# Optimization experiments

Measured on AMD Instinct MI355X. Metric: run time of the kernel, lower is better.

Reference implementation:

```python
import jax, jax.numpy as jnp
import numpy as np

CH = 64
HEADS = 4
HD = CH // HEADS          # 16
BLOCK = 8
HALO = 1
NEIGH = BLOCK + 2 * HALO  # 10
SR = 2
HDH = HD // 2             # 8


def conv1x1(x, w, b=None):
    y = jnp.einsum('oc,bchw->bohw', w, x)
    return y if b is None else y + b[None, :, None, None]


def dw3x3(x, w, pad_mode):
    # depthwise 3x3 conv, padding=1 with given pad mode
    xp = jnp.pad(x, ((0, 0), (0, 0), (1, 1), (1, 1)), mode=pad_mode)
    return jax.lax.conv_general_dilated(
        xp, w, (1, 1), 'VALID',
        dimension_numbers=('NCHW', 'OIHW', 'NCHW'),
        feature_group_count=x.shape[1])


def maxpool2(x):
    return jax.lax.reduce_window(x, -jnp.inf, jax.lax.max, (1, 1, 2, 2), (1, 1, 2, 2), 'VALID')


def l2norm(x):
    return x / jnp.maximum(jnp.linalg.norm(x, axis=-1, keepdims=True), 1e-12)


def sorted_channel_indices(q):
    # correlation-based channel ordering (computed under no_grad in torch)
    B, C = q.shape[0], q.shape[1]
    f = jax.lax.stop_gradient(q.reshape(B, C, -1))
    cen = f - f.mean(axis=2, keepdims=True)
    cov = jnp.einsum('bcn,bdn->bcd', cen, cen)
    std = jnp.sqrt(jnp.diagonal(cov, axis1=1, axis2=2) + 1e-8)
    denom = jnp.maximum(std[:, :, None] * std[:, None, :], 1e-8)
    sim = (cov / denom).mean(axis=2)
    return jnp.argsort(-sim, axis=1)  # descending


def up_bilinear_ac(x, s):
    # bilinear upsample, align_corners=True (torch convention)
    def lerp_axis(t, axis):
        n_in = t.shape[axis]
        n_out = n_in * s
        c = jnp.arange(n_out, dtype=t.dtype) * ((n_in - 1.0) / (n_out - 1.0))
        lo = jnp.clip(jnp.floor(c).astype(jnp.int32), 0, n_in - 2)
        w = c - lo.astype(t.dtype)
        shape = [1] * t.ndim
        shape[axis] = n_out
        w = w.reshape(shape)
        return jnp.take(t, lo, axis=axis) * (1 - w) + jnp.take(t, lo + 1, axis=axis) * w
    return lerp_axis(lerp_axis(x, 2), 3)


def _forward(x, qkv_w, lce_w, gate_w, gate_b, temp, rel_h_emb, rel_w_emb,
             down_w, down_b, up_w, up_b, gating_w, gating_b, proj_w, lp_w, lp_b):
    x_in = maxpool2(x)                         # sr=2 sampler
    B, C, H, W = x_in.shape                    # H,W divisible by BLOCK -> no pad branch
    hb, wb = H // BLOCK, W // BLOCK
    BL = B * hb * wb

    qkv = dw3x3(conv1x1(x_in, qkv_w), lce_w, 'constant')   # qkv_conv + lce
    q, k, v = jnp.split(qkv, 3, axis=1)

    idx = sorted_channel_indices(q)
    gidx = idx[:, :, None, None]
    q_s = jnp.take_along_axis(q, gidx, axis=1)
    k_s = jnp.take_along_axis(k, gidx, axis=1)
    v_s = jnp.take_along_axis(v, gidx, axis=1)

    # gating: grouped 1x1 conv, one [HD,HD] matmul per head
    qh = q_s.reshape(B, HEADS, HD, H, W)
    gate_score = jnp.einsum('goc,bgcxy->bgoxy', gate_w, qh) + gate_b[None, :, :, None, None]

    # query blocks: [BL, heads, block*block, hd]
    qi = qh.reshape(B, HEADS, HD, hb, BLOCK, wb, BLOCK)
    qi = qi.transpose(0, 3, 5, 1, 4, 6, 2).reshape(BL, HEADS, BLOCK * BLOCK, HD)

    def halo_patches(t):
        # F.unfold(kernel=NEIGH, stride=BLOCK, padding=HALO), zero pad
        tp = jnp.pad(t, ((0, 0), (0, 0), (HALO, HALO), (HALO, HALO)))
        ridx = jnp.arange(hb)[:, None] * BLOCK + jnp.arange(NEIGH)[None, :]
        cidx = jnp.arange(wb)[:, None] * BLOCK + jnp.arange(NEIGH)[None, :]
        p = tp[:, :, ridx, :][..., cidx]       # [B, C, hb, NEIGH, wb, NEIGH]
        p = p.reshape(B, HEADS, HD, hb, NEIGH, wb, NEIGH).transpose(0, 3, 5, 1, 4, 6, 2)
        return p.reshape(BL, HEADS, NEIGH, NEIGH, HD)

    ks = halo_patches(k_s)
    vi = halo_patches(v_s).reshape(BL, HEADS, NEIGH * NEIGH, HD)

    # relative positional embeddings on split key channels
    kh = ks[..., :HDH] + rel_h_emb             # [BL,heads,NEIGH,NEIGH,HDH]
    kw = ks[..., HDH:] + rel_w_emb
    ki = jnp.concatenate([kh, kw], axis=-1).reshape(BL, HEADS, NEIGH * NEIGH, HD)

    logits = jnp.einsum('bhqc,bhkc->bhqk', l2norm(qi), l2norm(ki)) * jnp.exp(temp)
    attn = jax.nn.softmax(logits, axis=-1)
    out_i = jnp.einsum('bhqk,bhkc->bhqc', attn, vi)

    out = out_i.reshape(B, hb, wb, HEADS, BLOCK, BLOCK, HD)
    out = out.transpose(0, 3, 6, 1, 4, 2, 5).reshape(B, HEADS, HD, H, W)
    out = (out * jax.nn.sigmoid(gate_score)).reshape(B, C, H, W)

    cache = q_s + k_s
    inv = jnp.argsort(idx, axis=1)[:, :, None, None]
    out = jnp.take_along_axis(out, inv, axis=1)
    cache = jnp.take_along_axis(cache, inv, axis=1)

    # Intra_CacheModulation
    mixed = out + cache
    g = jax.nn.gelu(conv1x1(mixed, gating_w, gating_b), approximate=False) * mixed
    out = out + conv1x1(conv1x1(g, down_w, down_b), up_w, up_b)

    out = conv1x1(out, proj_w)
    # LocalProp: depthwise 3x3 reflect-pad conv + bilinear x2 (align_corners=True)
    out = dw3x3(out, lp_w, 'reflect') + lp_b[None, :, None, None]
    out = up_bilinear_ac(out, SR)
    # final F.interpolate to input size is identity here (shapes already match)
    return out


def setup_inputs() -> dict:
    key = jax.random.key(0)
    ks = jax.random.split(key, 12)
    B, H, W = 4, 256, 256
    p = lambda k, shape, s=0.02: jax.random.normal(k, shape, jnp.float32) * s
    return {
        'x': jax.random.normal(ks[0], (B, CH, H, W), jnp.float32),
        'qkv_w': p(ks[1], (3 * CH, CH), 0.05),
        'lce_w': p(ks[2], (3 * CH, 1, 3, 3), 0.1),
        'gate_w': p(ks[3], (HEADS, HD, HD), 0.1),
        'gate_b': jnp.ones((HEADS, HD), jnp.float32),
        'temp': jnp.zeros((1, HEADS, 1, 1), jnp.float32),
        'rel_h_emb': p(ks[4], (1, HEADS, NEIGH, 1, HDH)),
        'rel_w_emb': p(ks[5], (1, HEADS, 1, NEIGH, HD - HDH)),
        'down_w': p(ks[6], (CH // 2, CH), 0.05),
        'down_b': jnp.zeros((CH // 2,), jnp.float32),
        'up_w': p(ks[7], (CH, CH // 2), 0.05),
        'up_b': jnp.zeros((CH,), jnp.float32),
        'gating_w': p(ks[8], (CH, CH), 0.05),
        'gating_b': jnp.zeros((CH,), jnp.float32),
        'proj_w': p(ks[9], (CH, CH), 0.05),
        'lp_w': p(ks[10], (CH, 1, 3, 3), 0.1),
        'lp_b': jnp.zeros((CH,), jnp.float32),
    }


def reference(x, qkv_w, lce_w, gate_w, gate_b, temp, rel_h_emb, rel_w_emb,
              down_w, down_b, up_w, up_b, gating_w, gating_b, proj_w, lp_w, lp_b):
    return _forward(x, qkv_w, lce_w, gate_w, gate_b, temp, rel_h_emb, rel_w_emb,
                    down_w, down_b, up_w, up_b, gating_w, gating_b, proj_w, lp_w, lp_b)
```

## Files before the change

kernel.cpp:

```cpp
#include <hip/hip_runtime.h>
#include <math.h>

#define HWP 16384

typedef float f32x2 __attribute__((ext_vector_type(2)));
typedef float f32x4 __attribute__((ext_vector_type(4)));

static __device__ __forceinline__ f32x2 pk_fma(f32x2 a, f32x2 b, f32x2 c) {
  f32x2 d;
  asm("v_pk_fma_f32 %0, %1, %2, %3" : "=v"(d) : "v"(a), "v"(b), "v"(c));
  return d;
}

static const size_t PRE_OFF  = 0;
static const size_t QKV_OFF  = 12582912;
static const size_t WT_OFF   = QKV_OFF;
static const size_t COVP_OFF = 0;
static const size_t MEAN_OFF = 2097152;
static const size_t COVS_OFF = 2097408;
static const size_t ATTN_OFF = 0;
static const size_t OUT3_OFF = 4194304;
static const size_t IDX_OFF  = 12570112;
static const size_t INV_OFF  = 12570368;
static const size_t GT2_OFF  = 12570624;
static const size_t DT2_OFF  = 12574720;
static const size_t UT2_OFF  = 12576768;
static const size_t PT2_OFF  = 12578816;

__global__ __launch_bounds__(256) void k_prep_wt(
    const float* __restrict__ qkv_w, float* __restrict__ wT) {
  int i = blockIdx.x * 256 + threadIdx.x;
  int o = i >> 6, c = i & 63;
  wT[c * 192 + o] = qkv_w[i];
}

__global__ __launch_bounds__(256) void k_prep2(
    const float* __restrict__ gating_w, const float* __restrict__ down_w,
    const float* __restrict__ up_w, const float* __restrict__ proj_w,
    float* __restrict__ gT, float* __restrict__ dT,
    float* __restrict__ uT, float* __restrict__ pT) {
  int t = blockIdx.x * 256 + threadIdx.x;
  if (t < 4096) {
    int o = t >> 6, d = t & 63;
    gT[d * 64 + o] = gating_w[t];
    pT[d * 64 + o] = proj_w[t];
  }
  if (t < 2048) {
    int o = t >> 6, d = t & 63;
    dT[d * 32 + o] = down_w[t];
    int o2 = t >> 5, d2 = t & 31;
    uT[d2 * 64 + o2] = up_w[t];
  }
}

__global__ __launch_bounds__(256) void k_pool_conv(
    const float* __restrict__ x, const float* __restrict__ wT,
    float* __restrict__ pre) {
  int b = blockIdx.x >> 8;
  int pix0 = (blockIdx.x & 255) * 64;
  __shared__ float xt[64 * 64];
  int t = threadIdx.x;
  for (int i = 0; i < 8; ++i) {
    int f = i * 256 + t;
    int c = f >> 5, pp = (f & 31) * 2;
    int pix = pix0 + pp;
    int y = pix >> 7, xx = pix & 127;
    const float* src = x + ((size_t)(b * 64 + c) * 65536) + (2 * y) * 256 + 2 * xx;
    float4 r0 = *(const float4*)src;
    float4 r1 = *(const float4*)(src + 256);
    xt[c * 64 + pp]     = fmaxf(fmaxf(r0.x, r0.y), fmaxf(r1.x, r1.y));
    xt[c * 64 + pp + 1] = fmaxf(fmaxf(r0.z, r0.w), fmaxf(r1.z, r1.w));
  }
  __syncthreads();
  int p = t & 63;
  int obase = __builtin_amdgcn_readfirstlane((t >> 6) * 48);
  const float* wbase = wT + obase;
  float acc[48];
#pragma unroll
  for (int j = 0; j < 48; ++j) acc[j] = 0.f;
  for (int c = 0; c < 64; ++c) {
    float xv = xt[c * 64 + p];
    const float* wc = wbase + c * 192;
#pragma unroll
    for (int j = 0; j < 48; ++j) acc[j] = fmaf(wc[j], xv, acc[j]);
  }
  float* dst = pre + ((size_t)b * 192 + obase) * HWP + pix0 + p;
#pragma unroll
  for (int j = 0; j < 48; ++j) dst[(size_t)j * HWP] = acc[j];
}

__global__ __launch_bounds__(256) void k_dw3x3_zero(
    const float* __restrict__ pre, const float* __restrict__ lce_w,
    float* __restrict__ qkv) {
  int gid = blockIdx.x * 256 + threadIdx.x;
  int c4 = gid & 31;
  int y  = (gid >> 5) & 127;
  int bc = gid >> 12;
  int ch = bc % 192;
  int x0 = c4 * 4;
  const float* base = pre + (size_t)bc * HWP;
  const float* w = lce_w + ch * 9;
  const float4 z4 = make_float4(0.f, 0.f, 0.f, 0.f);
  bool ym = y > 0, yp = y < 127;
  bool xl = x0 > 0, xr = x0 < 124;
  const float* rowm = base + (y - 1) * 128;
  const float* rowc = base + y * 128;
  const float* rowp = base + (y + 1) * 128;
  float4 vm = ym ? *(const float4*)(rowm + x0) : z4;
  float  lm = (ym && xl) ? rowm[x0 - 1] : 0.f;
  float  rm = (ym && xr) ? rowm[x0 + 4] : 0.f;
  float4 vc = *(const float4*)(rowc + x0);
  float  lc = xl ? rowc[x0 - 1] : 0.f;
  float  rc = xr ? rowc[x0 + 4] : 0.f;
  float4 vp = yp ? *(const float4*)(rowp + x0) : z4;
  float  lp = (yp && xl) ? rowp[x0 - 1] : 0.f;
  float  rp = (yp && xr) ? rowp[x0 + 4] : 0.f;
  float w0 = w[0], w1 = w[1], w2 = w[2], w3 = w[3], w4 = w[4],
        w5 = w[5], w6 = w[6], w7 = w[7], w8 = w[8];
  float4 o;
  o.x = fmaf(w8, vp.y, fmaf(w7, vp.x, fmaf(w6, lp,
        fmaf(w5, vc.y, fmaf(w4, vc.x, fmaf(w3, lc,
        fmaf(w2, vm.y, fmaf(w1, vm.x, fmaf(w0, lm, 0.f)))))))));
  o.y = fmaf(w8, vp.z, fmaf(w7, vp.y, fmaf(w6, vp.x,
        fmaf(w5, vc.z, fmaf(w4, vc.y, fmaf(w3, vc.x,
        fmaf(w2, vm.z, fmaf(w1, vm.y, fmaf(w0, vm.x, 0.f)))))))));
  o.z = fmaf(w8, vp.w, fmaf(w7, vp.z, fmaf(w6, vp.y,
        fmaf(w5, vc.w, fmaf(w4, vc.z, fmaf(w3, vc.y,
        fmaf(w2, vm.w, fmaf(w1, vm.z, fmaf(w0, vm.y, 0.f)))))))));
  o.w = fmaf(w8, rp,   fmaf(w7, vp.w, fmaf(w6, vp.z,
        fmaf(w5, rc,   fmaf(w4, vc.w, fmaf(w3, vc.z,
        fmaf(w2, rm,   fmaf(w1, vm.w, fmaf(w0, vm.z, 0.f)))))))));
  *(float4*)(qkv + (size_t)bc * HWP + y * 128 + x0) = o;
}

__global__ __launch_bounds__(256) void k_mean(
    const float* __restrict__ qkv, float* __restrict__ mean) {
  int bc = blockIdx.x;
  int b = bc >> 6, c = bc & 63;
  const float* src = qkv + ((size_t)b * 192 + c) * HWP;
  float s = 0.f;
  for (int i = threadIdx.x; i < HWP; i += 256) s += src[i];
  __shared__ float red[4];
  for (int off = 32; off > 0; off >>= 1) s += __shfl_down(s, off);
  int t = threadIdx.x;
  if ((t & 63) == 0) red[t >> 6] = s;
  __syncthreads();
  if (t == 0) mean[bc] = (red[0] + red[1] + red[2] + red[3]) * (1.f / 16384.f);
}

__global__ __launch_bounds__(256) void k_covpart(
    const float* __restrict__ qkv, const float* __restrict__ mean,
    float* __restrict__ covp) {
  int blk = blockIdx.x;
  int b = blk >> 7, chunk = blk & 127;
  int e0 = chunk * 128;
  __shared__ float qc[64 * 129];
  int t = threadIdx.x;
  for (int i = 0; i < 32; ++i) {
    int f = i * 256 + t;
    int c = f >> 7, e = f & 127;
    qc[c * 129 + e] = qkv[((size_t)b * 192 + c) * HWP + e0 + e] - mean[b * 64 + c];
  }
  __syncthreads();
  int d = t & 63;
  int crow = t >> 6;
  float acc[16];
#pragma unroll
  for (int i = 0; i < 16; ++i) acc[i] = 0.f;
  for (int e = 0; e < 128; ++e) {
    float qd = qc[d * 129 + e];
#pragma unroll
    for (int i = 0; i < 16; ++i) {
      int c = crow + 4 * i;
      acc[i] = fmaf(qc[c * 129 + e], qd, acc[i]);
    }
  }
  float* dst = covp + (size_t)blk * 4096;
#pragma unroll
  for (int i = 0; i < 16; ++i) {
    int c = crow + 4 * i;
    dst[c * 64 + d] = acc[i];
  }
}

__global__ __launch_bounds__(256) void k_covred(
    const float* __restrict__ covp, float* __restrict__ covs) {
  int blk = blockIdx.x;
  int b = blk >> 4;
  int pp = (blk & 15) * 256 + threadIdx.x;
  const float* src = covp + (size_t)b * 524288 + pp;
  float s = 0.f;
  for (int ch = 0; ch < 128; ++ch) s += src[ch * 4096];
  covs[b * 4096 + pp] = s;
}

__global__ __launch_bounds__(256) void k_simsort(
    const float* __restrict__ covs_g, int* __restrict__ idx, int* __restrict__ inv) {
  int b = blockIdx.x;
  __shared__ float covs[4096];
  __shared__ float stds[64];
  __shared__ float sims[64];
  int t = threadIdx.x;
  for (int i = 0; i < 16; ++i) covs[i * 256 + t] = covs_g[b * 4096 + i * 256 + t];
  __syncthreads();
  if (t < 64) stds[t] = sqrtf(covs[t * 64 + t] + 1e-8f);
  __syncthreads();
  if (t < 64) {
    float s = 0.f;
    float sc = stds[t];
    for (int d2 = 0; d2 < 64; ++d2) {
      float denom = fmaxf(sc * stds[d2], 1e-8f);
      s += covs[d2 * 64 + t] / denom;
    }
    sims[t] = s * (1.f / 64.f);
  }
  __syncthreads();
  if (t < 64) {
    float sv = sims[t];
    int r = 0;
    for (int d2 = 0; d2 < 64; ++d2) {
      float o = sims[d2];
      if (o > sv || (o == sv && d2 < t)) r++;
    }
    idx[b * 64 + r] = t;
    inv[b * 64 + t] = r;
  }
}

#define KVP 20
__global__ __launch_bounds__(128) void k_attn(
    const float* __restrict__ qkv, const int* __restrict__ idx,
    const float* __restrict__ rel_h, const float* __restrict__ rel_w,
    const float* __restrict__ gate_w, const float* __restrict__ gate_b,
    const float* __restrict__ temp, float* __restrict__ attn_out) {
  int bi = blockIdx.x;
  int head = bi & 3;
  int wj = (bi >> 2) & 15;
  int hi = (bi >> 6) & 15;
  int b = bi >> 10;
  int tt = threadIdx.x;
  int t = tt & 63;
  int w = __builtin_amdgcn_readfirstlane(tt >> 6);
  __shared__ __align__(16) float smem[2 * 100 * KVP];
  float* kr = smem;
  float* vr = smem + 100 * KVP;
  const size_t bb = (size_t)b * 192 * HWP;
  int chg[16];
#pragma unroll
  for (int ch = 0; ch < 16; ++ch) chg[ch] = idx[b * 64 + head * 16 + ch];
  if (tt < 100) {
    int py = tt / 10, px = tt - py * 10;
    int ky = hi * 8 + py - 1, kx = wj * 8 + px - 1;
    bool ok = (ky >= 0) && (ky < 128) && (kx >= 0) && (kx < 128);
    int sp = ky * 128 + kx;
    float kv[16];
    float s = 0.f;
#pragma unroll
    for (int ch = 0; ch < 16; ++ch) {
      float k = ok ? qkv[bb + (size_t)(64 + chg[ch]) * HWP + sp] : 0.f;
      k += (ch < 8) ? rel_h[(head * 10 + py) * 8 + ch]
                    : rel_w[(head * 10 + px) * 8 + (ch - 8)];
      kv[ch] = k;
      s += k * k;
    }
    float rn = 1.f / fmaxf(sqrtf(s), 1e-12f);
    float4* krow = (float4*)(kr + tt * KVP);
    krow[0] = make_float4(kv[0] * rn,  kv[1] * rn,  kv[2] * rn,  kv[3] * rn);
    krow[1] = make_float4(kv[4] * rn,  kv[5] * rn,  kv[6] * rn,  kv[7] * rn);
    krow[2] = make_float4(kv[8] * rn,  kv[9] * rn,  kv[10] * rn, kv[11] * rn);
    krow[3] = make_float4(kv[12] * rn, kv[13] * rn, kv[14] * rn, kv[15] * rn);
    float vv[16];
#pragma unroll
    for (int ch = 0; ch < 16; ++ch)
      vv[ch] = ok ? qkv[bb + (size_t)(128 + chg[ch]) * HWP + sp] : 0.f;
    float4* vrow = (float4*)(vr + tt * KVP);
    vrow[0] = make_float4(vv[0],  vv[1],  vv[2],  vv[3]);
    vrow[1] = make_float4(vv[4],  vv[5],  vv[6],  vv[7]);
    vrow[2] = make_float4(vv[8],  vv[9],  vv[10], vv[11]);
    vrow[3] = make_float4(vv[12], vv[13], vv[14], vv[15]);
  }
  int qy = hi * 8 + (t >> 3), qx = wj * 8 + (t & 7);
  float q[16];
  float qs = 0.f;
#pragma unroll
  for (int ch = 0; ch < 16; ++ch) {
    q[ch] = qkv[bb + (size_t)chg[ch] * HWP + qy * 128 + qx];
    qs += q[ch] * q[ch];
  }
  float T = expf(temp[head]);
  float qnT = T / fmaxf(sqrtf(qs), 1e-12f);
  f32x2 q2[8];
#pragma unroll
  for (int j = 0; j < 8; ++j) { q2[j].x = q[2 * j]; q2[j].y = q[2 * j + 1]; }
  __syncthreads();
  const f32x2 zz = {0.f, 0.f};
  f32x2 o2[8];
#pragma unroll
  for (int j = 0; j < 8; ++j) o2[j] = zz;
  float wsum = 0.f;
  for (int pyl = 0; pyl < 5; ++pyl) {
    int py = w * 5 + pyl;
    const float* kp0 = kr + py * 10 * KVP;
    const float* vp0 = vr + py * 10 * KVP;
    for (int px = 0; px < 10; ++px) {
      const f32x4* kp4 = (const f32x4*)(kp0 + px * KVP);
      const f32x4* vp4 = (const f32x4*)(vp0 + px * KVP);
      f32x4 kA = kp4[0], kB = kp4[1], kC = kp4[2], kD = kp4[3];
      f32x4 vA = vp4[0], vB = vp4[1], vC = vp4[2], vD = vp4[3];
      f32x2 dd0 = q2[0] * kA.xy;
      f32x2 dd1 = q2[1] * kA.zw;
      f32x2 dd2 = q2[2] * kB.xy;
      f32x2 dd3 = q2[3] * kB.zw;
      dd0 = pk_fma(q2[4], kC.xy, dd0);
      dd1 = pk_fma(q2[5], kC.zw, dd1);
      dd2 = pk_fma(q2[6], kD.xy, dd2);
      dd3 = pk_fma(q2[7], kD.zw, dd3);
      f32x2 dsA = dd0 + dd1;
      f32x2 dsB = dd2 + dd3;
      f32x2 dsC = dsA + dsB;
      float dacc = dsC.x + dsC.y;
      float e = __expf(fmaf(dacc, qnT, -T));
      wsum += e;
      f32x2 e2; e2.x = e; e2.y = e;
      o2[0] = pk_fma(e2, vA.xy, o2[0]);
      o2[1] = pk_fma(e2, vA.zw, o2[1]);
      o2[2] = pk_fma(e2, vB.xy, o2[2]);
      o2[3] = pk_fma(e2, vB.zw, o2[3]);
      o2[4] = pk_fma(e2, vC.xy, o2[4]);
      o2[5] = pk_fma(e2, vC.zw, o2[5]);
      o2[6] = pk_fma(e2, vD.xy, o2[6]);
      o2[7] = pk_fma(e2, vD.zw, o2[7]);
    }
  }
  __syncthreads();
  float* po = smem;
  float* pwp = smem + 2048;
  pwp[w * 64 + t] = wsum;
#pragma unroll
  for (int j = 0; j < 8; ++j) {
    po[(w * 16 + 2 * j) * 64 + t]     = o2[j].x;
    po[(w * 16 + 2 * j + 1) * 64 + t] = o2[j].y;
  }
  __syncthreads();
  float winv = 1.f / (pwp[t] + pwp[64 + t]);
  int ob = w * 8;
#pragma unroll
  for (int i = 0; i < 8; ++i) {
    int o = ob + i;
    float oc = po[o * 64 + t] + po[(16 + o) * 64 + t];
    float gsv = gate_b[head * 16 + o];
#pragma unroll
    for (int c = 0; c < 16; ++c)
      gsv = fmaf(gate_w[head * 256 + o * 16 + c], q[c], gsv);
    float sig = 1.f / (1.f + __expf(-gsv));
    attn_out[((size_t)b * 64 + chg[o]) * HWP + qy * 128 + qx] = oc * winv * sig;
  }
}

__global__ __launch_bounds__(256) void k_post(
    const float* __restrict__ attn, const float* __restrict__ qkv,
    const float* __restrict__ gT, const float* __restrict__ gating_b,
    const float* __restrict__ dT, const float* __restrict__ down_b,
    const float* __restrict__ uT, const float* __restrict__ up_b,
    const float* __restrict__ pT, float* __restrict__ out3) {
  __shared__ float xs[64 * 64];
  int t = threadIdx.x;
  int lane = t & 63;
  int w = t >> 6;
  int p = blockIdx.x * 64 + lane;
  int b = p >> 14;
  int pix = p & 16383;
  const float* ap = attn + (size_t)b * 64 * HWP + pix;
  const float* qp = qkv + (size_t)b * 192 * HWP + pix;
  float* op = out3 + (size_t)b * 64 * HWP + pix;
  int ob16 = __builtin_amdgcn_readfirstlane(w * 16);
  int ob8  = __builtin_amdgcn_readfirstlane(w * 8);
#pragma unroll
  for (int i = 0; i < 16; ++i) {
    int c = ob16 + i;
    xs[c * 64 + lane] = ap[(size_t)c * HWP] + qp[(size_t)c * HWP] + qp[(size_t)(64 + c) * HWP];
  }
  __syncthreads();
  {
    float acc[16];
#pragma unroll
    for (int o = 0; o < 16; ++o) acc[o] = gating_b[ob16 + o];
    for (int d = 0; d < 64; ++d) {
      float xv = xs[d * 64 + lane];
      const float* wd = gT + d * 64 + ob16;
#pragma unroll
      for (int o = 0; o < 16; ++o) acc[o] = fmaf(wd[o], xv, acc[o]);
    }
    __syncthreads();
#pragma unroll
    for (int o = 0; o < 16; ++o) {
      float a = acc[o];
      float ge = 0.5f * a * (1.f + erff(a * 0.70710678118654752f));
      xs[(ob16 + o) * 64 + lane] = ge * xs[(ob16 + o) * 64 + lane];
    }
    __syncthreads();
  }
  {
    float acc[8];
#pragma unroll
    for (int o = 0; o < 8; ++o) acc[o] = down_b[ob8 + o];
    for (int d = 0; d < 64; ++d) {
      float xv = xs[d * 64 + lane];
      const float* wd = dT + d * 32 + ob8;
#pragma unroll
      for (int o = 0; o < 8; ++o) acc[o] = fmaf(wd[o], xv, acc[o]);
    }
    __syncthreads();
#pragma unroll
    for (int o = 0; o < 8; ++o) xs[(ob8 + o) * 64 + lane] = acc[o];
    __syncthreads();
  }
  {
    float acc[16];
#pragma unroll
    for (int o = 0; o < 16; ++o) acc[o] = up_b[ob16 + o];
    for (int d = 0; d < 32; ++d) {
      float xv = xs[d * 64 + lane];
      const float* wd = uT + d * 64 + ob16;
#pragma unroll
      for (int o = 0; o < 16; ++o) acc[o] = fmaf(wd[o], xv, acc[o]);
    }
    __syncthreads();
#pragma unroll
    for (int o = 0; o < 16; ++o)
      xs[(ob16 + o) * 64 + lane] = acc[o] + ap[(size_t)(ob16 + o) * HWP];
    __syncthreads();
  }
  {
    float acc[16];
#pragma unroll
    for (int o = 0; o < 16; ++o) acc[o] = 0.f;
    for (int d = 0; d < 64; ++d) {
      float xv = xs[d * 64 + lane];
      const float* wd = pT + d * 64 + ob16;
#pragma unroll
      for (int o = 0; o < 16; ++o) acc[o] = fmaf(wd[o], xv, acc[o]);
    }
#pragma unroll
    for (int o = 0; o < 16; ++o) op[(size_t)(ob16 + o) * HWP] = acc[o];
  }
}

__global__ __launch_bounds__(256) void k_final(
    const float* __restrict__ out3, const float* __restrict__ lp_w,
    const float* __restrict__ lp_b, float* __restrict__ out) {
  int bi = blockIdx.x;
  int rt = bi & 7;
  int bc = bi >> 3;
  int ch = bc & 63;
  int r0 = rt * 16;
  __shared__ __align__(16) float tin[20 * 128];
  __shared__ __align__(16) float tdw[18 * 128];
  int t = threadIdx.x;
  const float* src = out3 + (size_t)bc * HWP;
  for (int i = 0; i < 3; ++i) {
    int f = i * 256 + t;
    if (f < 640) {
      int r = f >> 5, x4 = (f & 31) * 4;
      int ry = r0 - 2 + r;
      ry = ry < 0 ? -ry : (ry > 127 ? 254 - ry : ry);
      *(float4*)(tin + r * 128 + x4) = *(const float4*)(src + ry * 128 + x4);
    }
  }
  __syncthreads();
  float w0 = lp_w[ch * 9 + 0], w1 = lp_w[ch * 9 + 1], w2 = lp_w[ch * 9 + 2];
  float w3 = lp_w[ch * 9 + 3], w4 = lp_w[ch * 9 + 4], w5 = lp_w[ch * 9 + 5];
  float w6 = lp_w[ch * 9 + 6], w7 = lp_w[ch * 9 + 7], w8 = lp_w[ch * 9 + 8];
  float bias = lp_b[ch];
  for (int i = 0; i < 9; ++i) {
    int f = i * 256 + t;
    int r = f >> 7, xx = f & 127;
    int xm = (xx == 0) ? 1 : xx - 1;
    int xp = (xx == 127) ? 126 : xx + 1;
    const float* r0p = tin + r * 128;
    const float* r1p = r0p + 128;
    const float* r2p = r1p + 128;
    float acc = bias;
    acc = fmaf(w0, r0p[xm], acc); acc = fmaf(w1, r0p[xx], acc); acc = fmaf(w2, r0p[xp], acc);
    acc = fmaf(w3, r1p[xm], acc); acc = fmaf(w4, r1p[xx], acc); acc = fmaf(w5, r1p[xp], acc);
    acc = fmaf(w6, r2p[xm], acc); acc = fmaf(w7, r2p[xx], acc); acc = fmaf(w8, r2p[xp], acc);
    tdw[f] = acc;
  }
  __syncthreads();
  const float s = (float)(127.0 / 255.0);
  float* dst = out + (size_t)bc * 65536;
  for (int i = 0; i < 8; ++i) {
    int f = i * 256 + t;
    int vr = f >> 6, vx4 = (f & 63) * 4;
    int v = 2 * r0 + vr;
    float cy = (float)v * s;
    int ly = (int)floorf(cy); if (ly > 126) ly = 126;
    float wy = cy - (float)ly;
    int lr = ly - r0 + 1;
    const float* trow0 = tdw + lr * 128;
    const float* trow1 = trow0 + 128;
    float4 ov;
#pragma unroll
    for (int j = 0; j < 4; ++j) {
      int vx = vx4 + j;
      float cx = (float)vx * s;
      int lx = (int)floorf(cx); if (lx > 126) lx = 126;
      float wx = cx - (float)lx;
      float a  = trow0[lx];
      float bq = trow0[lx + 1];
      float c2 = trow1[lx];
      float d2 = trow1[lx + 1];
      float t0 = a  * (1.f - wy) + c2 * wy;
      float t1 = bq * (1.f - wy) + d2 * wy;
      (&ov.x)[j] = t0 * (1.f - wx) + t1 * wx;
    }
    *(float4*)(dst + v * 256 + vx4) = ov;
  }
}

extern "C" void kernel_launch(void* const* d_in, const int* in_sizes, int n_in,
                              void* d_out, int out_size, void* d_ws, size_t ws_size,
                              hipStream_t stream) {
  (void)in_sizes; (void)n_in; (void)out_size; (void)ws_size;
  const float* x        = (const float*)d_in[0];
  const float* qkv_w    = (const float*)d_in[1];
  const float* lce_w    = (const float*)d_in[2];
  const float* gate_w   = (const float*)d_in[3];
  const float* gate_b   = (const float*)d_in[4];
  const float* temp     = (const float*)d_in[5];
  const float* rel_h    = (const float*)d_in[6];
  const float* rel_w    = (const float*)d_in[7];
  const float* down_w   = (const float*)d_in[8];
  const float* down_b   = (const float*)d_in[9];
  const float* up_w     = (const float*)d_in[10];
  const float* up_b     = (const float*)d_in[11];
  const float* gating_w = (const float*)d_in[12];
  const float* gating_b = (const float*)d_in[13];
  const float* proj_w   = (const float*)d_in[14];
  const float* lp_w     = (const float*)d_in[15];
  const float* lp_b     = (const float*)d_in[16];
  float* fws = (float*)d_ws;
  float* outp = (float*)d_out;

  float* pre  = fws + PRE_OFF;
  float* qkv  = fws + QKV_OFF;
  float* attn = fws + ATTN_OFF;
  float* out3 = fws + OUT3_OFF;
  float* covp = fws + COVP_OFF;
  float* mean = fws + MEAN_OFF;
  int* idx = (int*)(fws + IDX_OFF);
  int* inv = (int*)(fws + INV_OFF);
  float* covs = fws + COVS_OFF;
  float* wT   = fws + WT_OFF;
  float* gT   = fws + GT2_OFF;
  float* dT   = fws + DT2_OFF;
  float* uT   = fws + UT2_OFF;
  float* pT   = fws + PT2_OFF;

  k_prep_wt<<<48, 256, 0, stream>>>(qkv_w, wT);
  k_pool_conv<<<1024, 256, 0, stream>>>(x, wT, pre);
  k_dw3x3_zero<<<12288, 256, 0, stream>>>(pre, lce_w, qkv);
  k_prep2<<<16, 256, 0, stream>>>(gating_w, down_w, up_w, proj_w, gT, dT, uT, pT);
  k_mean<<<256, 256, 0, stream>>>(qkv, mean);
  k_covpart<<<512, 256, 0, stream>>>(qkv, mean, covp);
  k_covred<<<64, 256, 0, stream>>>(covp, covs);
  k_simsort<<<4, 256, 0, stream>>>(covs, idx, inv);
  k_attn<<<4096, 128, 0, stream>>>(qkv, idx, rel_h, rel_w, gate_w, gate_b, temp, attn);
  k_post<<<1024, 256, 0, stream>>>(attn, qkv, gT, gating_b, dT, down_b,
                                   uT, up_b, pT, out3);
  k_final<<<2048, 256, 0, stream>>>(out3, lp_w, lp_b, outp);
  (void)inv;
}
```

Measured before the change: 360.1 us.

## Run attention block as a single wavefront over all 100 neighbours

Measured after the change: 368.8 us. 2.4% more time.

```diff
diff --git a/kernel.cpp b/kernel.cpp
--- a/kernel.cpp
+++ b/kernel.cpp
@@ -228,7 +228,7 @@
 }
 
 #define KVP 20
-__global__ __launch_bounds__(128) void k_attn(
+__global__ __launch_bounds__(64) void k_attn(
     const float* __restrict__ qkv, const int* __restrict__ idx,
     const float* __restrict__ rel_h, const float* __restrict__ rel_w,
     const float* __restrict__ gate_w, const float* __restrict__ gate_b,
@@ -238,9 +238,7 @@
   int wj = (bi >> 2) & 15;
   int hi = (bi >> 6) & 15;
   int b = bi >> 10;
-  int tt = threadIdx.x;
-  int t = tt & 63;
-  int w = __builtin_amdgcn_readfirstlane(tt >> 6);
+  int t = threadIdx.x;
   __shared__ __align__(16) float smem[2 * 100 * KVP];
   float* kr = smem;
   float* vr = smem + 100 * KVP;
@@ -248,36 +246,40 @@
   int chg[16];
 #pragma unroll
   for (int ch = 0; ch < 16; ++ch) chg[ch] = idx[b * 64 + head * 16 + ch];
-  if (tt < 100) {
-    int py = tt / 10, px = tt - py * 10;
-    int ky = hi * 8 + py - 1, kx = wj * 8 + px - 1;
-    bool ok = (ky >= 0) && (ky < 128) && (kx >= 0) && (kx < 128);
-    int sp = ky * 128 + kx;
-    float kv[16];
-    float s = 0.f;
-#pragma unroll
-    for (int ch = 0; ch < 16; ++ch) {
-      float k = ok ? qkv[bb + (size_t)(64 + chg[ch]) * HWP + sp] : 0.f;
-      k += (ch < 8) ? rel_h[(head * 10 + py) * 8 + ch]
-                    : rel_w[(head * 10 + px) * 8 + (ch - 8)];
-      kv[ch] = k;
-      s += k * k;
-    }
-    float rn = 1.f / fmaxf(sqrtf(s), 1e-12f);
-    float4* krow = (float4*)(kr + tt * KVP);
-    krow[0] = make_float4(kv[0] * rn,  kv[1] * rn,  kv[2] * rn,  kv[3] * rn);
-    krow[1] = make_float4(kv[4] * rn,  kv[5] * rn,  kv[6] * rn,  kv[7] * rn);
-    krow[2] = make_float4(kv[8] * rn,  kv[9] * rn,  kv[10] * rn, kv[11] * rn);
-    krow[3] = make_float4(kv[12] * rn, kv[13] * rn, kv[14] * rn, kv[15] * rn);
-    float vv[16];
-#pragma unroll
-    for (int ch = 0; ch < 16; ++ch)
-      vv[ch] = ok ? qkv[bb + (size_t)(128 + chg[ch]) * HWP + sp] : 0.f;
-    float4* vrow = (float4*)(vr + tt * KVP);
-    vrow[0] = make_float4(vv[0],  vv[1],  vv[2],  vv[3]);
-    vrow[1] = make_float4(vv[4],  vv[5],  vv[6],  vv[7]);
-    vrow[2] = make_float4(vv[8],  vv[9],  vv[10], vv[11]);
-    vrow[3] = make_float4(vv[12], vv[13], vv[14], vv[15]);
+#pragma unroll
+  for (int pass = 0; pass < 2; ++pass) {
+    int pos = pass * 64 + t;
+    if (pos < 100) {
+      int py = pos / 10, px = pos - py * 10;
+      int ky = hi * 8 + py - 1, kx = wj * 8 + px - 1;
+      bool ok = (ky >= 0) && (ky < 128) && (kx >= 0) && (kx < 128);
+      int sp = ky * 128 + kx;
+      float kv[16];
+      float s = 0.f;
+#pragma unroll
+      for (int ch = 0; ch < 16; ++ch) {
+        float k = ok ? qkv[bb + (size_t)(64 + chg[ch]) * HWP + sp] : 0.f;
+        k += (ch < 8) ? rel_h[(head * 10 + py) * 8 + ch]
+                      : rel_w[(head * 10 + px) * 8 + (ch - 8)];
+        kv[ch] = k;
+        s += k * k;
+      }
+      float rn = 1.f / fmaxf(sqrtf(s), 1e-12f);
+      float4* krow = (float4*)(kr + pos * KVP);
+      krow[0] = make_float4(kv[0] * rn,  kv[1] * rn,  kv[2] * rn,  kv[3] * rn);
+      krow[1] = make_float4(kv[4] * rn,  kv[5] * rn,  kv[6] * rn,  kv[7] * rn);
+      krow[2] = make_float4(kv[8] * rn,  kv[9] * rn,  kv[10] * rn, kv[11] * rn);
+      krow[3] = make_float4(kv[12] * rn, kv[13] * rn, kv[14] * rn, kv[15] * rn);
+      float vv[16];
+#pragma unroll
+      for (int ch = 0; ch < 16; ++ch)
+        vv[ch] = ok ? qkv[bb + (size_t)(128 + chg[ch]) * HWP + sp] : 0.f;
+      float4* vrow = (float4*)(vr + pos * KVP);
+      vrow[0] = make_float4(vv[0],  vv[1],  vv[2],  vv[3]);
+      vrow[1] = make_float4(vv[4],  vv[5],  vv[6],  vv[7]);
+      vrow[2] = make_float4(vv[8],  vv[9],  vv[10], vv[11]);
+      vrow[3] = make_float4(vv[12], vv[13], vv[14], vv[15]);
+    }
   }
   int qy = hi * 8 + (t >> 3), qx = wj * 8 + (t & 7);
   float q[16];
@@ -292,19 +294,17 @@
   f32x2 q2[8];
 #pragma unroll
   for (int j = 0; j < 8; ++j) { q2[j].x = q[2 * j]; q2[j].y = q[2 * j + 1]; }
-  __syncthreads();
   const f32x2 zz = {0.f, 0.f};
   f32x2 o2[8];
 #pragma unroll
   for (int j = 0; j < 8; ++j) o2[j] = zz;
   float wsum = 0.f;
-  for (int pyl = 0; pyl < 5; ++pyl) {
-    int py = w * 5 + pyl;
-    const float* kp0 = kr + py * 10 * KVP;
-    const float* vp0 = vr + py * 10 * KVP;
-    for (int px = 0; px < 10; ++px) {
-      const f32x4* kp4 = (const f32x4*)(kp0 + px * KVP);
-      const f32x4* vp4 = (const f32x4*)(vp0 + px * KVP);
+  {
+    const float* kp = kr;
+    const float* vp = vr;
+    for (int kk = 0; kk < 100; ++kk) {
+      const f32x4* kp4 = (const f32x4*)kp;
+      const f32x4* vp4 = (const f32x4*)vp;
       f32x4 kA = kp4[0], kB = kp4[1], kC = kp4[2], kD = kp4[3];
       f32x4 vA = vp4[0], vB = vp4[1], vC = vp4[2], vD = vp4[3];
       f32x2 dd0 = q2[0] * kA.xy;
@@ -330,30 +330,22 @@
       o2[5] = pk_fma(e2, vC.zw, o2[5]);
       o2[6] = pk_fma(e2, vD.xy, o2[6]);
       o2[7] = pk_fma(e2, vD.zw, o2[7]);
-    }
-  }
-  __syncthreads();
-  float* po = smem;
-  float* pwp = smem + 2048;
-  pwp[w * 64 + t] = wsum;
-#pragma unroll
-  for (int j = 0; j < 8; ++j) {
-    po[(w * 16 + 2 * j) * 64 + t]     = o2[j].x;
-    po[(w * 16 + 2 * j + 1) * 64 + t] = o2[j].y;
-  }
-  __syncthreads();
-  float winv = 1.f / (pwp[t] + pwp[64 + t]);
-  int ob = w * 8;
-#pragma unroll
-  for (int i = 0; i < 8; ++i) {
-    int o = ob + i;
-    float oc = po[o * 64 + t] + po[(16 + o) * 64 + t];
+      kp += KVP;
+      vp += KVP;
+    }
+  }
+  float winv = 1.f / wsum;
+  float out[16];
+#pragma unroll
+  for (int j = 0; j < 8; ++j) { out[2 * j] = o2[j].x; out[2 * j + 1] = o2[j].y; }
+#pragma unroll
+  for (int o = 0; o < 16; ++o) {
     float gsv = gate_b[head * 16 + o];
 #pragma unroll
     for (int c = 0; c < 16; ++c)
       gsv = fmaf(gate_w[head * 256 + o * 16 + c], q[c], gsv);
     float sig = 1.f / (1.f + __expf(-gsv));
-    attn_out[((size_t)b * 64 + chg[o]) * HWP + qy * 128 + qx] = oc * winv * sig;
+    attn_out[((size_t)b * 64 + chg[o]) * HWP + qy * 128 + qx] = out[o] * winv * sig;
   }
 }
 
@@ -565,7 +557,7 @@
   k_covpart<<<512, 256, 0, stream>>>(qkv, mean, covp);
   k_covred<<<64, 256, 0, stream>>>(covp, covs);
   k_simsort<<<4, 256, 0, stream>>>(covs, idx, inv);
-  k_attn<<<4096, 128, 0, stream>>>(qkv, idx, rel_h, rel_w, gate_w, gate_b, temp, attn);
+  k_attn<<<4096, 64, 0, stream>>>(qkv, idx, rel_h, rel_w, gate_w, gate_b, temp, attn);
   k_post<<<1024, 256, 0, stream>>>(attn, qkv, gT, gating_b, dT, down_b,
                                    uT, up_b, pT, out3);
   k_final<<<2048, 256, 0, stream>>>(out3, lp_w, lp_b, outp);
```
